# Kernel tuning notes

Hardware: AMD Instinct MI355X
Metric: run time of the kernel (lower is better)

The kernel has to match this reference:

```python
import jax, jax.numpy as jnp
import numpy as np

N = 100000
E = 1600000
IN_DIM = 128
HID = 16      # per-head dim
HEADS = 4
FEAT = HID * HEADS  # 64
OUT_DIM = 64
EPS = 0.5
LAYERS = 2


def setup_inputs() -> dict:
    key = jax.random.key(0)
    ks = jax.random.split(key, 8)
    return {
        "h": jax.random.normal(ks[0], (N, IN_DIM), dtype=jnp.float32),
        "src": jax.random.randint(ks[1], (E,), 0, N, dtype=jnp.int64),
        "dst": jax.random.randint(ks[2], (E,), 0, N, dtype=jnp.int64),
        "t1_W": jax.random.normal(ks[3], (IN_DIM, FEAT), dtype=jnp.float32) * 0.1,
        "t1_b": jnp.zeros((FEAT,), dtype=jnp.float32),
        "t2_W": jax.random.normal(ks[4], (FEAT, OUT_DIM), dtype=jnp.float32) * 0.1,
        "t2_b": jnp.zeros((OUT_DIM,), dtype=jnp.float32),
        "gate_W": jax.random.normal(ks[5], (LAYERS, 2 * HID, 1), dtype=jnp.float32) * 0.2,
        "gate_b": jnp.zeros((LAYERS, 1), dtype=jnp.float32),
    }


def reference(h, src, dst, t1_W, t1_b, t2_W, t2_b, gate_W, gate_b):
    # t1 + relu
    x = jax.nn.relu(h @ t1_W + t1_b)            # [N, FEAT]
    raw = x

    # symmetric degree norm: deg^-0.5 from in-degrees (clamped at 1)
    deg = jax.ops.segment_sum(jnp.ones((E,), x.dtype), dst, num_segments=N)
    norm = jnp.clip(deg, 1.0, None) ** -0.5     # [N]

    xh = x.reshape(N, HEADS, HID)
    edge_norm = norm[dst] * norm[src]           # [E]
    h1 = raw
    # NOTE: original forward never updates x inside the loop; each layer
    # consumes the same relu(t1(h)) and only the last layer's h0 survives.
    for l in range(LAYERS):
        hs = xh[src]                            # [E, H, D] gather src
        hd = xh[dst]                            # [E, H, D] gather dst
        hcat = jnp.concatenate([hd, hs], axis=-1)  # [E, H, 2D]
        s = jnp.tanh(hcat @ gate_W[l] + gate_b[l])[..., 0]  # [E, H]
        s = s * edge_norm[:, None]
        e_h = (hs * s[..., None]).reshape(E, FEAT)          # [E, FEAT]
        h0 = jax.ops.segment_sum(e_h, dst, num_segments=N)  # scatter-sum
        h1 = EPS * raw + h0

    return h1 @ t2_W + t2_b                      # [N, OUT_DIM]
```

## Files before the change

### kernel.cpp

```cpp
#include <hip/hip_runtime.h>
#include <hip/hip_fp16.h>
#include <math.h>

#define N_NODES 100000
#define E_EDGES 1600000
#define IN_DIM  128
#define FEAT    64
#define OUT_DIM 64
#define NBKT    391
#define CAP     6144
#define RNG     4096
#define NSCB    ((E_EDGES + RNG - 1) / RNG)
#define G1B     ((N_NODES + 255) / 256)

typedef float vfloat2 __attribute__((ext_vector_type(2)));

__global__ __launch_bounds__(256) void k_binscatter(
    const int* __restrict__ src, const int* __restrict__ dst,
    int* __restrict__ bucket_cursor, int* __restrict__ binned)
{
    __shared__ int hist[NBKT];
    __shared__ int baseS[NBKT];
    __shared__ int cursor[NBKT];
    __shared__ int gbase[NBKT];
    __shared__ int sA[512], sB[512];
    __shared__ int buf[RNG];
    __shared__ unsigned short bkt[RNG];

    const int tid  = threadIdx.x;
    const int e0   = blockIdx.x * RNG;
    const int ecnt = min(RNG, E_EDGES - e0);

    for (int i = tid; i < NBKT; i += 256) hist[i] = 0;
    __syncthreads();

    int dsave[16];
#pragma unroll
    for (int k = 0; k < 16; ++k) {
        int e = e0 + k * 256 + tid;
        int d = (e < E_EDGES) ? dst[e] : -1;
        dsave[k] = d;
        if (d >= 0) atomicAdd(&hist[d >> 8], 1);
    }
    __syncthreads();

    for (int i = tid; i < 512; i += 256) sA[i] = (i < NBKT) ? hist[i] : 0;
    __syncthreads();
    int* pa = sA; int* pb = sB;
    for (int off = 1; off < 512; off <<= 1) {
        for (int i = tid; i < 512; i += 256)
            pb[i] = pa[i] + ((i >= off) ? pa[i - off] : 0);
        __syncthreads();
        int* t = pa; pa = pb; pb = t;
    }
    for (int i = tid; i < NBKT; i += 256) {
        int ex = pa[i] - hist[i];
        baseS[i]  = ex;
        cursor[i] = ex;
    }
    __syncthreads();

#pragma unroll
    for (int k = 0; k < 16; ++k) {
        int d = dsave[k];
        if (d >= 0) {
            int e   = e0 + k * 256 + tid;
            int s   = src[e];
            int b   = d >> 8;
            int pos = atomicAdd(&cursor[b], 1);
            buf[pos] = ((d & 255) << 17) | s;
            bkt[pos] = (unsigned short)b;
        }
    }
    __syncthreads();

    for (int t = tid; t < NBKT; t += 256) {
        int cnt = hist[t];
        int g   = cnt ? atomicAdd(&bucket_cursor[t], cnt) : 0;
        gbase[t] = g - baseS[t];
    }
    __syncthreads();

    for (int i = tid; i < ecnt; i += 256) {
        int b   = bkt[i];
        int off = gbase[b] + i;
        if (off < CAP) binned[b * CAP + off] = buf[i];
    }
}

__global__ __launch_bounds__(256) void k_bucketfinal(
    const int* __restrict__ binned, const int* __restrict__ bucket_cursor,
    int* __restrict__ deg, int* __restrict__ rowptr, int* __restrict__ src_sorted)
{
    __shared__ int sA[512], sB[512];
    __shared__ int hist[256];
    __shared__ int scn[256];
    __shared__ int cur[256];
    const int b   = blockIdx.x;
    const int tid = threadIdx.x;

    for (int i = tid; i < 512; i += 256) sA[i] = (i < NBKT) ? bucket_cursor[i] : 0;
    __syncthreads();
    int* pa = sA; int* pb = sB;
    for (int off = 1; off < 512; off <<= 1) {
        for (int i = tid; i < 512; i += 256)
            pb[i] = pa[i] + ((i >= off) ? pa[i - off] : 0);
        __syncthreads();
        int* t = pa; pa = pb; pb = t;
    }
    const int cnt  = bucket_cursor[b];
    const int eb   = pa[b] - cnt;
    const int base = b * CAP;
    __syncthreads();

    hist[tid] = 0;
    __syncthreads();
    for (int i = tid; i < cnt; i += 256)
        atomicAdd(&hist[binned[base + i] >> 17], 1);
    __syncthreads();

    int v = hist[tid];
    scn[tid] = v;
    __syncthreads();
    for (int off = 1; off < 256; off <<= 1) {
        int add = (tid >= off) ? scn[tid - off] : 0;
        __syncthreads();
        scn[tid] += add;
        __syncthreads();
    }
    int ex = scn[tid] - v;
    cur[tid] = ex;
    int n = b * 256 + tid;
    if (n < N_NODES) {
        deg[n]    = v;
        rowptr[n] = eb + ex;
    }
    if (b == 0 && tid == 0) rowptr[N_NODES] = E_EDGES;
    __syncthreads();

    for (int i = tid; i < cnt; i += 256) {
        int p   = binned[base + i];
        int dl  = p >> 17;
        int pos = atomicAdd(&cur[dl], 1);
        src_sorted[eb + pos] = p & 0x1FFFF;
    }
}

__global__ __launch_bounds__(256, 3) void k_gemm1(
    const float* __restrict__ h, const float* __restrict__ W1,
    const float* __restrict__ b1, const int* __restrict__ deg,
    const float* __restrict__ gate_W,
    __half* __restrict__ xs2h, unsigned int* __restrict__ xq,
    float* __restrict__ aproj, float* __restrict__ bproj)
{
    __shared__ float Ws[IN_DIM * FEAT];
    __shared__ float hT[16 * 260];
    const int tid = threadIdx.x;
    const int r0  = blockIdx.x * 256;

    for (int i = tid; i < IN_DIM * FEAT / 4; i += 256)
        ((float4*)Ws)[i] = ((const float4*)W1)[i];

    const int rg = tid >> 2;
    const int cg = tid & 3;
    const int c0 = cg * 16;
    float acc[4][16];
#pragma unroll
    for (int i = 0; i < 4; ++i)
#pragma unroll
        for (int j = 0; j < 16; ++j) acc[i][j] = 0.f;

    const int  myrow = r0 + tid;
    const bool rok   = myrow < N_NODES;

    for (int kc = 0; kc < IN_DIM / 16; ++kc) {
        float4 f[4];
        if (rok) {
            const float4* hp = (const float4*)(h + (size_t)myrow * IN_DIM + kc * 16);
            f[0] = hp[0]; f[1] = hp[1]; f[2] = hp[2]; f[3] = hp[3];
        } else {
            f[0] = f[1] = f[2] = f[3] = make_float4(0.f, 0.f, 0.f, 0.f);
        }
        __syncthreads();
#pragma unroll
        for (int q = 0; q < 4; ++q) {
            hT[(q * 4 + 0) * 260 + tid] = f[q].x;
            hT[(q * 4 + 1) * 260 + tid] = f[q].y;
            hT[(q * 4 + 2) * 260 + tid] = f[q].z;
            hT[(q * 4 + 3) * 260 + tid] = f[q].w;
        }
        __syncthreads();
#pragma unroll
        for (int kk = 0; kk < 16; ++kk) {
            float4 a4 = *(const float4*)&hT[kk * 260 + rg * 4];
            const float* wrow = &Ws[(kc * 16 + kk) * FEAT + c0];
            float4 w0 = ((const float4*)wrow)[0];
            float4 w1 = ((const float4*)wrow)[1];
            float4 w2 = ((const float4*)wrow)[2];
            float4 w3 = ((const float4*)wrow)[3];
            const float a[4] = {a4.x, a4.y, a4.z, a4.w};
            const float w[16] = {w0.x, w0.y, w0.z, w0.w, w1.x, w1.y, w1.z, w1.w,
                                 w2.x, w2.y, w2.z, w2.w, w3.x, w3.y, w3.z, w3.w};
#pragma unroll
            for (int i = 0; i < 4; ++i)
#pragma unroll
                for (int j = 0; j < 16; ++j)
                    acc[i][j] = fmaf(a[i], w[j], acc[i][j]);
        }
    }

#pragma unroll
    for (int i = 0; i < 4; ++i) {
        int r = r0 + rg * 4 + i;
        if (r >= N_NODES) continue;
        float nr = rsqrtf(fmaxf((float)deg[r], 1.f));
        float xa = 0.f, xb = 0.f;
        alignas(16) __half hv[16];
        float vs[16];
#pragma unroll
        for (int j = 0; j < 16; ++j) {
            float v = acc[i][j] + b1[c0 + j];
            v = v > 0.f ? v : 0.f;
            xa = fmaf(v, gate_W[32 + j], xa);
            xb = fmaf(v, gate_W[48 + j], xb);
            float sv = v * nr;
            vs[j] = sv;
            hv[j] = __float2half(sv);
        }
        float4* xp = (float4*)(xs2h + (size_t)r * FEAT + c0);
        xp[0] = *(const float4*)&hv[0];
        xp[1] = *(const float4*)&hv[8];
        unsigned int u[4];
#pragma unroll
        for (int q = 0; q < 4; ++q) {
            unsigned int t = 0;
            t = __builtin_amdgcn_cvt_pk_fp8_f32(vs[q*4+0], vs[q*4+1], t, false);
            t = __builtin_amdgcn_cvt_pk_fp8_f32(vs[q*4+2], vs[q*4+3], t, true);
            u[q] = t;
        }
        ((uint4*)xq)[(size_t)r * 4 + cg] = make_uint4(u[0], u[1], u[2], u[3]);
        aproj[(size_t)r * 4 + cg] = xa;
        bproj[(size_t)r * 4 + cg] = xb;
    }
}

__global__ __launch_bounds__(256) void k_aggregate(
    const uint4* __restrict__ xq4, const __half2* __restrict__ xs2h2,
    const float* __restrict__ aproj, const float* __restrict__ bproj,
    const int* __restrict__ rowptr, const int* __restrict__ src_sorted,
    const float* __restrict__ gate_b, float* __restrict__ v_out)
{
    const int tid    = threadIdx.x;
    const int lane   = tid & 63;
    const int e      = lane >> 2;
    const int l4     = lane & 3;
    const int wave   = blockIdx.x * 4 + (tid >> 6);
    const int nwaves = gridDim.x * 4;
    const float gb   = gate_b[1];
    const float C    = 2.8853900817779268f;

    for (int n = wave; n < N_NODES; n += nwaves) {
        const int beg = rowptr[n];
        const int end = rowptr[n + 1];
        const int cnt = end - beg;
        const float a_d = aproj[(size_t)n * 4 + l4] + gb;

        float acc[16];
#pragma unroll
        for (int k = 0; k < 16; ++k) acc[k] = 0.f;

        if (cnt > 0) {
            const int last = end - 1;
            int  j0  = beg + e;
            bool ok0 = j0 < end;
            int  s0  = src_sorted[ok0 ? j0 : last];
            uint4 x0 = xq4[(size_t)s0 * 4 + l4];
            float b0 = bproj[(size_t)s0 * 4 + l4];
            int  j1  = j0 + 16;
            bool ok1 = j1 < end;
            int  s1  = src_sorted[ok1 ? j1 : last];

            for (int j = beg; j < end; j += 16) {
                const bool more = (j + 16) < end;
                uint4 x1 = make_uint4(0u, 0u, 0u, 0u);
                float b1 = 0.f;
                int   s2 = s1;
                bool  ok2 = false;
                if (more) {
                    x1 = xq4[(size_t)s1 * 4 + l4];
                    b1 = bproj[(size_t)s1 * 4 + l4];
                    int j2 = j + 32 + e;
                    ok2 = j2 < end;
                    s2 = src_sorted[ok2 ? j2 : last];
                }
                float ex = __builtin_amdgcn_exp2f(C * (a_d + b0));
                float t  = 1.f - 2.f * __builtin_amdgcn_rcpf(ex + 1.f);
                t = ok0 ? t : 0.f;
#pragma unroll
                for (int w = 0; w < 4; ++w) {
                    const unsigned int xw = ((const unsigned int*)&x0)[w];
                    vfloat2 lo = __builtin_amdgcn_cvt_pk_f32_fp8(xw, false);
                    vfloat2 hi = __builtin_amdgcn_cvt_pk_f32_fp8(xw, true);
                    acc[w * 4 + 0] = fmaf(t, lo[0], acc[w * 4 + 0]);
                    acc[w * 4 + 1] = fmaf(t, lo[1], acc[w * 4 + 1]);
                    acc[w * 4 + 2] = fmaf(t, hi[0], acc[w * 4 + 2]);
                    acc[w * 4 + 3] = fmaf(t, hi[1], acc[w * 4 + 3]);
                }
                if (more) {
                    x0 = x1; b0 = b1; ok0 = ok1; ok1 = ok2; s1 = s2;
                }
            }
        }

        const bool elo = (e & 1) == 0;
        float r8[8];
#pragma unroll
        for (int i = 0; i < 8; ++i) {
            float give = elo ? acc[8 + i] : acc[i];
            float got  = __shfl_xor(give, 4, 64);
            r8[i] = (elo ? acc[i] : acc[8 + i]) + got;
        }
        const bool e2lo = (e & 2) == 0;
        float v4[4];
#pragma unroll
        for (int i = 0; i < 4; ++i) {
            float give = e2lo ? r8[4 + i] : r8[i];
            float got  = __shfl_xor(give, 8, 64);
            v4[i] = (e2lo ? r8[i] : r8[4 + i]) + got;
        }
#pragma unroll
        for (int i = 0; i < 4; ++i) v4[i] += __shfl_xor(v4[i], 16, 64);
#pragma unroll
        for (int i = 0; i < 4; ++i) v4[i] += __shfl_xor(v4[i], 32, 64);

        const float dg = fmaxf((float)cnt, 1.f);
        const float nd = rsqrtf(dg);
        const float sd = dg * nd;

        if (e < 4) {
            const int q = ((e & 1) << 1) | ((e >> 1) & 1);
            const int Q = l4 * 4 + q;
            const __half2* hp = xs2h2 + (size_t)n * 32 + Q * 2;
            float2 fa = __half22float2(hp[0]);
            float2 fb = __half22float2(hp[1]);
            float4 v;
            v.x = fmaf(0.5f * sd, fa.x, v4[0] * nd);
            v.y = fmaf(0.5f * sd, fa.y, v4[1] * nd);
            v.z = fmaf(0.5f * sd, fb.x, v4[2] * nd);
            v.w = fmaf(0.5f * sd, fb.y, v4[3] * nd);
            ((float4*)v_out)[(size_t)n * 16 + Q] = v;
        }
    }
}

__global__ __launch_bounds__(256, 3) void k_gemm2(
    float* __restrict__ v, const float* __restrict__ W2, const float* __restrict__ b2)
{
    __shared__ float Ws[FEAT * OUT_DIM];
    __shared__ float vT[16 * 260];
    const int tid = threadIdx.x;
    const int r0  = blockIdx.x * 256;

    for (int i = tid; i < FEAT * OUT_DIM / 4; i += 256)
        ((float4*)Ws)[i] = ((const float4*)W2)[i];

    const int rg = tid >> 2;
    const int cg = tid & 3;
    const int c0 = cg * 16;
    float acc[4][16];
#pragma unroll
    for (int i = 0; i < 4; ++i)
#pragma unroll
        for (int j = 0; j < 16; ++j) acc[i][j] = 0.f;

    const int  myrow = r0 + tid;
    const bool rok   = myrow < N_NODES;

    for (int kc = 0; kc < FEAT / 16; ++kc) {
        float4 f[4];
        if (rok) {
            const float4* vp = (const float4*)(v + (size_t)myrow * FEAT + kc * 16);
            f[0] = vp[0]; f[1] = vp[1]; f[2] = vp[2]; f[3] = vp[3];
        } else {
            f[0] = f[1] = f[2] = f[3] = make_float4(0.f, 0.f, 0.f, 0.f);
        }
        __syncthreads();
#pragma unroll
        for (int q = 0; q < 4; ++q) {
            vT[(q * 4 + 0) * 260 + tid] = f[q].x;
            vT[(q * 4 + 1) * 260 + tid] = f[q].y;
            vT[(q * 4 + 2) * 260 + tid] = f[q].z;
            vT[(q * 4 + 3) * 260 + tid] = f[q].w;
        }
        __syncthreads();
#pragma unroll
        for (int kk = 0; kk < 16; ++kk) {
            float4 a4 = *(const float4*)&vT[kk * 260 + rg * 4];
            const float* wrow = &Ws[(kc * 16 + kk) * OUT_DIM + c0];
            float4 w0 = ((const float4*)wrow)[0];
            float4 w1 = ((const float4*)wrow)[1];
            float4 w2 = ((const float4*)wrow)[2];
            float4 w3 = ((const float4*)wrow)[3];
            const float a[4] = {a4.x, a4.y, a4.z, a4.w};
            const float w[16] = {w0.x, w0.y, w0.z, w0.w, w1.x, w1.y, w1.z, w1.w,
                                 w2.x, w2.y, w2.z, w2.w, w3.x, w3.y, w3.z, w3.w};
#pragma unroll
            for (int i = 0; i < 4; ++i)
#pragma unroll
                for (int j = 0; j < 16; ++j)
                    acc[i][j] = fmaf(a[i], w[j], acc[i][j]);
        }
    }

#pragma unroll
    for (int i = 0; i < 4; ++i) {
        int r = r0 + rg * 4 + i;
        if (r >= N_NODES) continue;
        float* op = &v[(size_t)r * OUT_DIM + c0];
#pragma unroll
        for (int q = 0; q < 4; ++q) {
            float4 o = make_float4(acc[i][q*4]   + b2[c0 + q*4],
                                   acc[i][q*4+1] + b2[c0 + q*4 + 1],
                                   acc[i][q*4+2] + b2[c0 + q*4 + 2],
                                   acc[i][q*4+3] + b2[c0 + q*4 + 3]);
            ((float4*)op)[q] = o;
        }
    }
}

extern "C" void kernel_launch(void* const* d_in, const int* in_sizes, int n_in,
                              void* d_out, int out_size, void* d_ws, size_t ws_size,
                              hipStream_t stream)
{
    const float* h   = (const float*)d_in[0];
    const int*   src = (const int*)d_in[1];
    const int*   dst = (const int*)d_in[2];
    const float* W1  = (const float*)d_in[3];
    const float* b1  = (const float*)d_in[4];
    const float* W2  = (const float*)d_in[5];
    const float* b2  = (const float*)d_in[6];
    const float* gW  = (const float*)d_in[7];
    const float* gb  = (const float*)d_in[8];
    float* out = (float*)d_out;

    int* bucket_cursor = (int*)d_ws;
    int* binned        = bucket_cursor + NBKT;
    int* src_sorted    = binned + (size_t)NBKT * CAP;
    int* rowptr        = src_sorted + E_EDGES;
    int* deg           = rowptr + (N_NODES + 1);
    float* aproj       = (float*)(deg + N_NODES);
    float* bproj       = aproj + (size_t)N_NODES * 4;
    __half* xs2h       = (__half*)(bproj + (size_t)N_NODES * 4);
    unsigned int* xq   = (unsigned int*)(xs2h + (size_t)N_NODES * FEAT);

    hipMemsetAsync(bucket_cursor, 0, NBKT * sizeof(int), stream);

    k_binscatter <<<NSCB, 256, 0, stream>>>(src, dst, bucket_cursor, binned);
    k_bucketfinal<<<NBKT, 256, 0, stream>>>(binned, bucket_cursor, deg, rowptr, src_sorted);
    k_gemm1      <<<G1B, 256, 0, stream>>>(h, W1, b1, deg, gW, xs2h, xq, aproj, bproj);
    k_aggregate  <<<2048, 256, 0, stream>>>((const uint4*)xq, (const __half2*)xs2h,
                                            aproj, bproj, rowptr, src_sorted, gb, out);
    k_gemm2      <<<G1B, 256, 0, stream>>>(out, W2, b2);
}
```

Before: 255.1 us.

## Fuse output projection GEMM into aggregation kernel epilogue

Removes the separate k_gemm2 kernel and computes the final 64x64 projection per node inside k_aggregate. W2 is staged in shared memory per block, and each wave writes its aggregated feature row to a small shared buffer before every lane computes one output column. This avoids writing and re-reading the intermediate node features through global memory and drops one launch. In exchange, each block uses more shared memory, which may lower occupancy, and the wave relies on implicit intra-wave ordering for the shared buffer.

Measured after the change: 247.5 us. -3.0%, faster.

```diff
diff --git a/kernel.cpp b/kernel.cpp
--- a/kernel.cpp
+++ b/kernel.cpp
@@ -248,16 +248,27 @@
     const uint4* __restrict__ xq4, const __half2* __restrict__ xs2h2,
     const float* __restrict__ aproj, const float* __restrict__ bproj,
     const int* __restrict__ rowptr, const int* __restrict__ src_sorted,
-    const float* __restrict__ gate_b, float* __restrict__ v_out)
+    const float* __restrict__ gate_b,
+    const float* __restrict__ W2, const float* __restrict__ b2,
+    float* __restrict__ out)
 {
+    __shared__ float W2s[FEAT * OUT_DIM];
+    __shared__ float vbuf[4][FEAT];
+
     const int tid    = threadIdx.x;
     const int lane   = tid & 63;
     const int e      = lane >> 2;
     const int l4     = lane & 3;
-    const int wave   = blockIdx.x * 4 + (tid >> 6);
+    const int wslot  = tid >> 6;
+    const int wave   = blockIdx.x * 4 + wslot;
     const int nwaves = gridDim.x * 4;
     const float gb   = gate_b[1];
     const float C    = 2.8853900817779268f;
+
+    for (int i = tid; i < FEAT * OUT_DIM / 4; i += 256)
+        ((float4*)W2s)[i] = ((const float4*)W2)[i];
+    const float myb2 = b2[lane];
+    __syncthreads();
 
     for (int n = wave; n < N_NODES; n += nwaves) {
         const int beg = rowptr[n];
@@ -348,83 +359,19 @@
             v.y = fmaf(0.5f * sd, fa.y, v4[1] * nd);
             v.z = fmaf(0.5f * sd, fb.x, v4[2] * nd);
             v.w = fmaf(0.5f * sd, fb.y, v4[3] * nd);
-            ((float4*)v_out)[(size_t)n * 16 + Q] = v;
-        }
-    }
-}
-
-__global__ __launch_bounds__(256, 3) void k_gemm2(
-    float* __restrict__ v, const float* __restrict__ W2, const float* __restrict__ b2)
-{
-    __shared__ float Ws[FEAT * OUT_DIM];
-    __shared__ float vT[16 * 260];
-    const int tid = threadIdx.x;
-    const int r0  = blockIdx.x * 256;
-
-    for (int i = tid; i < FEAT * OUT_DIM / 4; i += 256)
-        ((float4*)Ws)[i] = ((const float4*)W2)[i];
-
-    const int rg = tid >> 2;
-    const int cg = tid & 3;
-    const int c0 = cg * 16;
-    float acc[4][16];
-#pragma unroll
-    for (int i = 0; i < 4; ++i)
-#pragma unroll
-        for (int j = 0; j < 16; ++j) acc[i][j] = 0.f;
-
-    const int  myrow = r0 + tid;
-    const bool rok   = myrow < N_NODES;
-
-    for (int kc = 0; kc < FEAT / 16; ++kc) {
-        float4 f[4];
-        if (rok) {
-            const float4* vp = (const float4*)(v + (size_t)myrow * FEAT + kc * 16);
-            f[0] = vp[0]; f[1] = vp[1]; f[2] = vp[2]; f[3] = vp[3];
-        } else {
-            f[0] = f[1] = f[2] = f[3] = make_float4(0.f, 0.f, 0.f, 0.f);
-        }
-        __syncthreads();
-#pragma unroll
-        for (int q = 0; q < 4; ++q) {
-            vT[(q * 4 + 0) * 260 + tid] = f[q].x;
-            vT[(q * 4 + 1) * 260 + tid] = f[q].y;
-            vT[(q * 4 + 2) * 260 + tid] = f[q].z;
-            vT[(q * 4 + 3) * 260 + tid] = f[q].w;
-        }
-        __syncthreads();
-#pragma unroll
-        for (int kk = 0; kk < 16; ++kk) {
-            float4 a4 = *(const float4*)&vT[kk * 260 + rg * 4];
-            const float* wrow = &Ws[(kc * 16 + kk) * OUT_DIM + c0];
-            float4 w0 = ((const float4*)wrow)[0];
-            float4 w1 = ((const float4*)wrow)[1];
-            float4 w2 = ((const float4*)wrow)[2];
-            float4 w3 = ((const float4*)wrow)[3];
-            const float a[4] = {a4.x, a4.y, a4.z, a4.w};
-            const float w[16] = {w0.x, w0.y, w0.z, w0.w, w1.x, w1.y, w1.z, w1.w,
-                                 w2.x, w2.y, w2.z, w2.w, w3.x, w3.y, w3.z, w3.w};
-#pragma unroll
-            for (int i = 0; i < 4; ++i)
-#pragma unroll
-                for (int j = 0; j < 16; ++j)
-                    acc[i][j] = fmaf(a[i], w[j], acc[i][j]);
-        }
-    }
-
-#pragma unroll
-    for (int i = 0; i < 4; ++i) {
-        int r = r0 + rg * 4 + i;
-        if (r >= N_NODES) continue;
-        float* op = &v[(size_t)r * OUT_DIM + c0];
-#pragma unroll
-        for (int q = 0; q < 4; ++q) {
-            float4 o = make_float4(acc[i][q*4]   + b2[c0 + q*4],
-                                   acc[i][q*4+1] + b2[c0 + q*4 + 1],
-                                   acc[i][q*4+2] + b2[c0 + q*4 + 2],
-                                   acc[i][q*4+3] + b2[c0 + q*4 + 3]);
-            ((float4*)op)[q] = o;
-        }
+            *(float4*)&vbuf[wslot][Q * 4] = v;
+        }
+        float oacc = myb2;
+        const float* vb = vbuf[wslot];
+#pragma unroll
+        for (int fq = 0; fq < 16; ++fq) {
+            float4 vv = *(const float4*)&vb[fq * 4];
+            oacc = fmaf(vv.x, W2s[(fq * 4 + 0) * OUT_DIM + lane], oacc);
+            oacc = fmaf(vv.y, W2s[(fq * 4 + 1) * OUT_DIM + lane], oacc);
+            oacc = fmaf(vv.z, W2s[(fq * 4 + 2) * OUT_DIM + lane], oacc);
+            oacc = fmaf(vv.w, W2s[(fq * 4 + 3) * OUT_DIM + lane], oacc);
+        }
+        out[(size_t)n * OUT_DIM + lane] = oacc;
     }
 }
 
@@ -459,6 +406,6 @@
     k_bucketfinal<<<NBKT, 256, 0, stream>>>(binned, bucket_cursor, deg, rowptr, src_sorted);
     k_gemm1      <<<G1B, 256, 0, stream>>>(h, W1, b1, deg, gW, xs2h, xq, aproj, bproj);
     k_aggregate  <<<2048, 256, 0, stream>>>((const uint4*)xq, (const __half2*)xs2h,
-                                            aproj, bproj, rowptr, src_sorted, gb, out);
-    k_gemm2      <<<G1B, 256, 0, stream>>>(out, W2, b2);
+                                            aproj, bproj, rowptr, src_sorted, gb,
+                                            W2, b2, out);
 }
```
